# Optimization experiments

Measured on AMD Instinct MI355X. Metric: run time of the kernel, lower is better.

The kernel has to match this reference:

```python
import jax, jax.numpy as jnp
import numpy as np

N = 100000
IN_F, C1, C2, C3, OUT_F = 64, 64, 64, 64, 8


def setup_inputs() -> dict:
    key = jax.random.key(0)
    ks = jax.random.split(key, 12)
    x = jax.random.normal(ks[0], (N, IN_F), dtype=jnp.float32)
    edge_index = jax.random.randint(ks[1], (2, 1600000), 0, N, dtype=jnp.int64)

    def lin(kw, kb, fi, fo):
        s = 1.0 / np.sqrt(fi)
        W = jax.random.uniform(kw, (fi, fo), jnp.float32, -s, s)
        b = jax.random.uniform(kb, (fo,), jnp.float32, -s, s)
        return W, b

    W1, b1 = lin(ks[2], ks[3], IN_F, C1)
    W2, b2 = lin(ks[4], ks[5], C1, C2)
    W3, b3 = lin(ks[6], ks[7], C2, C3)
    Wl, bl = lin(ks[8], ks[9], C3, OUT_F)
    return {"x": x, "edge_index": edge_index, "W1": W1, "b1": b1,
            "W2": W2, "b2": b2, "W3": W3, "b3": b3, "Wl": Wl, "bl": bl}


def _gcn_norm(edge_index, n):
    # add self loops, compute symmetric normalization D^-1/2 A D^-1/2
    loops = jnp.arange(n, dtype=edge_index.dtype)
    src = jnp.concatenate([edge_index[0], loops])
    dst = jnp.concatenate([edge_index[1], loops])
    deg = jax.ops.segment_sum(jnp.ones_like(dst, dtype=jnp.float32), dst, num_segments=n)
    dis = jnp.where(deg > 0, jax.lax.rsqrt(deg), 0.0)
    norm = dis[src] * dis[dst]  # [E+N]
    return src, dst, norm


def _gcn_layer(h, W, b, src, dst, norm, n):
    h = h @ W                                   # [N, Fout] small GEMM
    msg = h[src] * norm[:, None]                # gather + scale, [E+N, Fout]
    agg = jax.ops.segment_sum(msg, dst, num_segments=n)  # scatter-add
    return agg + b


def reference(x, edge_index, W1, b1, W2, b2, W3, b3, Wl, bl):
    n = x.shape[0]
    src, dst, norm = _gcn_norm(edge_index, n)
    h = jax.nn.relu(_gcn_layer(x, W1, b1, src, dst, norm, n))
    h = jax.nn.relu(_gcn_layer(h, W2, b2, src, dst, norm, n))
    h = jax.nn.relu(_gcn_layer(h, W3, b3, src, dst, norm, n))
    return h @ Wl + bl
```

## Files before the change

kernel.cpp:

```cpp
#include <hip/hip_runtime.h>
#include <hip/hip_fp16.h>

#define F 64
#define CHUNK 2048
#define BN 512
#define BSHIFT 9
#define CAP 20480

typedef int v4i __attribute__((ext_vector_type(4)));
typedef float fx4 __attribute__((ext_vector_type(4)));
typedef float v2f __attribute__((ext_vector_type(2)));
typedef _Float16 h8f __attribute__((ext_vector_type(8)));

union FB8 { uint4 u; h8f h; };
union FX4P { fx4 v; v2f p[2]; };

__global__ __launch_bounds__(256) void k_blkcnt(const int* __restrict__ dst,
                                                int* __restrict__ blkcnt,
                                                int E, int NB, int NBKT) {
    __shared__ int lcnt[256];
    int b = blockIdx.x, t = threadIdx.x;
    lcnt[t] = 0;
    __syncthreads();
    const v4i* d4 = (const v4i*)dst;
    int g0 = (b * CHUNK) >> 2;
    int E4 = E >> 2;
#pragma unroll
    for (int k = 0; k < 2; ++k) {
        int gi = g0 + k * 256 + t;
        if (gi < E4) {
            v4i q = __builtin_nontemporal_load(d4 + gi);
            atomicAdd(&lcnt[q.x >> BSHIFT], 1);
            atomicAdd(&lcnt[q.y >> BSHIFT], 1);
            atomicAdd(&lcnt[q.z >> BSHIFT], 1);
            atomicAdd(&lcnt[q.w >> BSHIFT], 1);
        }
    }
    __syncthreads();
    if (t < NBKT) blkcnt[t * NB + b] = lcnt[t];
}

__global__ __launch_bounds__(256) void k_bktscan(const int* __restrict__ blkcnt,
                                                 int* __restrict__ blkoff,
                                                 int* __restrict__ bkttot, int NB) {
    __shared__ int s[256];
    __shared__ int running;
    int seg = blockIdx.x;
    int t = threadIdx.x;
    if (t == 0) running = 0;
    __syncthreads();
    for (int base = 0; base < NB; base += 256) {
        int i = base + t;
        int v = (i < NB) ? blkcnt[seg * NB + i] : 0;
        s[t] = v;
        __syncthreads();
        for (int off = 1; off < 256; off <<= 1) {
            int x = (t >= off) ? s[t - off] : 0;
            __syncthreads();
            s[t] += x;
            __syncthreads();
        }
        int rbase = running;
        if (i < NB) blkoff[seg * NB + i] = rbase + s[t] - v;
        int ctot = s[255];
        __syncthreads();
        if (t == 0) running = rbase + ctot;
        __syncthreads();
    }
    if (t == 0) bkttot[seg] = running;
}

__global__ void k_sb(const int* __restrict__ bkttot, int* __restrict__ sb, int NBKT) {
    __shared__ int s[256];
    int t = threadIdx.x;
    int v = (t < NBKT) ? bkttot[t] : 0;
    s[t] = v;
    __syncthreads();
    for (int off = 1; off < 256; off <<= 1) {
        int x = (t >= off) ? s[t - off] : 0;
        __syncthreads();
        s[t] += x;
        __syncthreads();
    }
    if (t < NBKT) sb[t] = s[t] - v;
    if (t == NBKT - 1) sb[NBKT] = s[t];
}

__global__ __launch_bounds__(256) void k_stage2(const int* __restrict__ src,
                                                const int* __restrict__ dst,
                                                const int* __restrict__ blkoff,
                                                const int* __restrict__ sb,
                                                unsigned* __restrict__ stage,
                                                int E, int NB, int NBKT) {
    __shared__ int lcnt[256];
    __shared__ int lbase[257];
    __shared__ int obase[256];
    __shared__ int s[256];
    __shared__ unsigned rec[CHUNK];
    __shared__ unsigned char binof[CHUNK];
    int b = blockIdx.x, t = threadIdx.x;
    lcnt[t] = 0;
    __syncthreads();
    const v4i* d4 = (const v4i*)dst;
    const v4i* s4 = (const v4i*)src;
    int g0 = (b * CHUNK) >> 2;
    int E4 = E >> 2;
    int myseg[8], myrank[8];
    unsigned myrec[8];
#pragma unroll
    for (int k = 0; k < 2; ++k) {
        int gi = g0 + k * 256 + t;
        bool ok = gi < E4;
        v4i qd = {0, 0, 0, 0}, qs = {0, 0, 0, 0};
        if (ok) {
            qd = __builtin_nontemporal_load(d4 + gi);
            qs = __builtin_nontemporal_load(s4 + gi);
        }
        int dd[4] = {qd.x, qd.y, qd.z, qd.w};
        int ss[4] = {qs.x, qs.y, qs.z, qs.w};
#pragma unroll
        for (int j = 0; j < 4; ++j) {
            int idx = k * 4 + j;
            myseg[idx] = -1;
            if (ok) {
                int sg = dd[j] >> BSHIFT;
                myseg[idx] = sg;
                myrank[idx] = atomicAdd(&lcnt[sg], 1);
                myrec[idx] = ((unsigned)(dd[j] & (BN - 1)) << 17) | (unsigned)ss[j];
            }
        }
    }
    __syncthreads();
    int v = lcnt[t];
    s[t] = v;
    __syncthreads();
    for (int off = 1; off < 256; off <<= 1) {
        int x = (t >= off) ? s[t - off] : 0;
        __syncthreads();
        s[t] += x;
        __syncthreads();
    }
    lbase[t] = s[t] - v;
    if (t == 255) lbase[256] = s[255];
    obase[t] = (t < NBKT) ? sb[t] + blkoff[t * NB + b] : 0;
    __syncthreads();
#pragma unroll
    for (int k = 0; k < 8; ++k) {
        if (myseg[k] >= 0) {
            int p = lbase[myseg[k]] + myrank[k];
            rec[p] = myrec[k];
            binof[p] = (unsigned char)myseg[k];
        }
    }
    __syncthreads();
    int tot = lbase[256];
    for (int j = t; j < tot; j += 256) {
        int sg = binof[j];
        stage[obase[sg] + (j - lbase[sg])] = rec[j];
    }
}

__global__ __launch_bounds__(1024) void k_bincount(const unsigned* __restrict__ stage,
                                                   const int* __restrict__ sb,
                                                   int* __restrict__ count,
                                                   float* __restrict__ dis,
                                                   int* __restrict__ padtot, int n) {
    __shared__ int lc[BN];
    int bkt = blockIdx.x, t = threadIdx.x;
    int nb0 = bkt << BSHIFT;
    if (t < BN) lc[t] = 0;
    __syncthreads();
    int r0 = sb[bkt], r1 = sb[bkt + 1];
    for (int j = r0 + t; j < r1; j += 1024) {
        unsigned r = stage[j];
        atomicAdd(&lc[r >> 17], 1);
    }
    __syncthreads();
    int pv = 0;
    if (t < BN) {
        int node = nb0 + t;
        int cv = lc[t];
        if (node < n) {
            count[node] = cv;
            dis[node] = rsqrtf((float)(cv + 1));
            pv = (cv + 3) & ~3;
        }
    }
    __syncthreads();
    if (t < BN) lc[t] = pv;
    __syncthreads();
    for (int off = 256; off > 0; off >>= 1) {
        if (t < off) lc[t] += lc[t + off];
        __syncthreads();
    }
    if (t == 0) padtot[bkt] = lc[0];
}

__global__ void k_sb2(const int* __restrict__ padtot, int* __restrict__ rbase,
                      int* __restrict__ row_start, int NBKT, int n) {
    __shared__ int s[256];
    int t = threadIdx.x;
    int v = (t < NBKT) ? padtot[t] : 0;
    s[t] = v;
    __syncthreads();
    for (int off = 1; off < 256; off <<= 1) {
        int x = (t >= off) ? s[t - off] : 0;
        __syncthreads();
        s[t] += x;
        __syncthreads();
    }
    if (t < NBKT) rbase[t] = s[t] - v;
    if (t == NBKT - 1) { rbase[NBKT] = s[t]; row_start[n] = s[t]; }
}

__global__ __launch_bounds__(512) void k_binfill(const unsigned* __restrict__ stage,
                                                 const int* __restrict__ sb,
                                                 const int* __restrict__ count,
                                                 const int* __restrict__ rbase,
                                                 int* __restrict__ row_start,
                                                 int* __restrict__ csr, int n) {
    __shared__ int lcur[BN];
    __shared__ int sc[BN];
    __shared__ int buf[CAP];
    int bkt = blockIdx.x, t = threadIdx.x;
    int nb0 = bkt << BSHIFT;
    int node = nb0 + t;
    int pv = (node < n) ? ((count[node] + 3) & ~3) : 0;
    sc[t] = pv;
    __syncthreads();
    for (int off = 1; off < BN; off <<= 1) {
        int x = (t >= off) ? sc[t - off] : 0;
        __syncthreads();
        sc[t] += x;
        __syncthreads();
    }
    int excl = sc[t] - pv;
    int w0 = rbase[bkt];
    int wlen = sc[BN - 1];
    lcur[t] = excl;
    if (node < n) row_start[node] = w0 + excl;
    for (int j = t; j < wlen && j < CAP; j += 512) buf[j] = n;
    __syncthreads();
    int r0 = sb[bkt], r1 = sb[bkt + 1];
    for (int j = r0 + t; j < r1; j += 512) {
        unsigned r = stage[j];
        int p = atomicAdd(&lcur[r >> 17], 1);
        if (p < CAP) buf[p] = (int)(r & 0x1FFFFu);
    }
    __syncthreads();
    for (int j = t; j < wlen && j < CAP; j += 512) csr[w0 + j] = buf[j];
}

__global__ void k_prep(const float4* __restrict__ x4, const float* __restrict__ dis,
                       uint2* __restrict__ hs, uint2* __restrict__ hs2, int n) {
    int i = blockIdx.x * blockDim.x + threadIdx.x;
    int tot = (n + 1) * 16;
    if (i < tot) {
        int row = i >> 4;
        float dv = 0.0f;
        float4 v = make_float4(0.f, 0.f, 0.f, 0.f);
        if (row < n) { dv = dis[row]; v = x4[i]; }
        __half2 h01 = __floats2half2_rn(dv * v.x, dv * v.y);
        __half2 h23 = __floats2half2_rn(dv * v.z, dv * v.w);
        uint2 u;
        u.x = *(unsigned*)&h01;
        u.y = *(unsigned*)&h23;
        hs[i] = u;
    } else if (i < tot + 16) {
        hs2[(size_t)n * 16 + (i - tot)] = make_uint2(0u, 0u);
    }
}

__global__ __launch_bounds__(256) void k_layer(const __half* __restrict__ hin,
        const float* __restrict__ W, const float* __restrict__ b,
        const int* __restrict__ row_start, const int* __restrict__ csr,
        const float* __restrict__ dis, __half* __restrict__ hout,
        int n, int scale_out) {
    __shared__ char lds_all[16384];
    int tid = threadIdx.x;
    int lane = tid & 63;
    int wv = tid >> 6;
    int r0 = (blockIdx.x * 4 + wv) << 4;
    if (r0 >= n) return;
    char* myLds = lds_all + (wv << 12);
    unsigned short* X16 = (unsigned short*)myLds;
    const uint4* h4 = (const uint4*)hin;

    int r_  = lane & 15;
    int g4  = lane >> 4;
    int q32 = lane >> 1;
    int c2  = lane & 1;

    int lo = row_start[r0 + r_];
    int hi = row_start[r0 + r_ + 1];
    int s0 = __shfl(lo, 0);
    int s4 = __shfl(hi, 15);
    int NBb = (s4 - s0 + 31) >> 5;
    unsigned deg = (unsigned)(hi - lo);

    fx4 acc0 = {0.f, 0.f, 0.f, 0.f};
    fx4 acc1 = acc0, acc2 = acc0, acc3 = acc0;

    auto getnode = [&](int i) -> int {
        if (i < NBb) {
            int slot = s0 + (i << 5) + q32;
            int nd = csr[slot];
            return (slot < s4) ? nd : n;
        }
        return (q32 < 16) ? (r0 + q32) : n;
    };

    int nd0 = getnode(0);
    int ba = nd0 * 8 + c2 * 4;
    uint4 G0 = h4[ba], G1 = h4[ba + 1], G2 = h4[ba + 2], G3 = h4[ba + 3];
    int ndn = getnode(1);

    int q0 = q32;
    int q1 = q32 ^ 8;
    int q2 = q32 ^ 16;
    int q3 = q32 ^ 24;

    for (int t = 0; t <= NBb; ++t) {
        int fb = c2 << 5;
#define PUT(J, GG) { \
    unsigned short* p = X16 + ((fb + 8 * (J)) << 5); \
    p[q0]       = (unsigned short)(GG.x); \
    p[32 + q0]  = (unsigned short)(GG.x >> 16); \
    p[64 + q1]  = (unsigned short)(GG.y); \
    p[96 + q1]  = (unsigned short)(GG.y >> 16); \
    p[128 + q2] = (unsigned short)(GG.z); \
    p[160 + q2] = (unsigned short)(GG.z >> 16); \
    p[192 + q3] = (unsigned short)(GG.w); \
    p[224 + q3] = (unsigned short)(GG.w >> 16); \
}
        PUT(0, G0) PUT(1, G1) PUT(2, G2) PUT(3, G3)
#undef PUT
        if (t < NBb) {
            int bb = ndn * 8 + c2 * 4;
            G0 = h4[bb]; G1 = h4[bb + 1]; G2 = h4[bb + 2]; G3 = h4[bb + 3];
            ndn = getnode(t + 2);
        }
        unsigned w[4];
        if (t < NBb) {
            unsigned u0 = (unsigned)(s0 + (t << 5) + (g4 << 3)) - (unsigned)lo;
#pragma unroll
            for (int jj = 0; jj < 4; ++jj)
                w[jj] = ((u0 + 2 * jj) < deg ? 0x3C00u : 0u) |
                        ((u0 + 2 * jj + 1) < deg ? 0x3C000000u : 0u);
        } else {
            int k0 = g4 << 3;
#pragma unroll
            for (int jj = 0; jj < 4; ++jj)
                w[jj] = ((k0 + 2 * jj) == r_ ? 0x3C00u : 0u) |
                        ((k0 + 2 * jj + 1) == r_ ? 0x3C000000u : 0u);
        }
        FB8 af; af.u = make_uint4(w[0], w[1], w[2], w[3]);
        const char* rb = myLds + ((r_ << 6) + ((g4 ^ ((r_ >> 1) & 3)) << 4));
        FB8 b0, b1, b2, b3;
        b0.u = *(const uint4*)(rb);
        b1.u = *(const uint4*)(rb + 1024);
        b2.u = *(const uint4*)(rb + 2048);
        b3.u = *(const uint4*)(rb + 3072);
        acc0 = __builtin_amdgcn_mfma_f32_16x16x32_f16(af.h, b0.h, acc0, 0, 0, 0);
        acc1 = __builtin_amdgcn_mfma_f32_16x16x32_f16(af.h, b1.h, acc1, 0, 0, 0);
        acc2 = __builtin_amdgcn_mfma_f32_16x16x32_f16(af.h, b2.h, acc2, 0, 0, 0);
        acc3 = __builtin_amdgcn_mfma_f32_16x16x32_f16(af.h, b3.h, acc3, 0, 0, 0);
    }

    float* T = (float*)myLds;
#define TSTORE(S, A) { \
    int fb_ = ((16 * (S) + r_) << 4) + (g4 << 2); \
    *(fx4*)(T + fb_) = A; }
    TSTORE(0, acc0) TSTORE(1, acc1) TSTORE(2, acc2) TSTORE(3, acc3)
#undef TSTORE

    float bb_ = b[lane];
    v2f yv2[8];
#pragma unroll
    for (int k = 0; k < 8; ++k) { yv2[k].x = 0.f; yv2[k].y = 0.f; }
    const float* Wp = W + lane;
#pragma unroll 4
    for (int f = 0; f < 64; ++f) {
        float w = Wp[f << 6];
        v2f wv; wv.x = w; wv.y = w;
        const float* Tf = T + (f << 4);
        FX4P d0, d1, d2, d3;
        d0.v = *(const fx4*)(Tf);
        d1.v = *(const fx4*)(Tf + 4);
        d2.v = *(const fx4*)(Tf + 8);
        d3.v = *(const fx4*)(Tf + 12);
        yv2[0] += d0.p[0] * wv;  yv2[1] += d0.p[1] * wv;
        yv2[2] += d1.p[0] * wv;  yv2[3] += d1.p[1] * wv;
        yv2[4] += d2.p[0] * wv;  yv2[5] += d2.p[1] * wv;
        yv2[6] += d3.p[0] * wv;  yv2[7] += d3.p[1] * wv;
    }

#pragma unroll
    for (int r = 0; r < 16; ++r) {
        float yvr = (r & 1) ? yv2[r >> 1].y : yv2[r >> 1].x;
        float dd = dis[r0 + r];
        float y = fmaxf(yvr * dd + bb_, 0.f);
        if (scale_out) y *= dd;
        hout[((size_t)(r0 + r) << 6) + lane] = __float2half(y);
    }
}

__global__ __launch_bounds__(256) void k_final(const __half* __restrict__ h,
                                               const float* __restrict__ Wl,
                                               const float* __restrict__ bl,
                                               float* __restrict__ out, int n) {
    __shared__ float Ws[F * 8];
    __shared__ float bs[8];
    int tid = threadIdx.x;
    Ws[tid] = Wl[tid];
    Ws[tid + 256] = Wl[tid + 256];
    if (tid < 8) bs[tid] = bl[tid];
    __syncthreads();
    int idx = blockIdx.x * 256 + tid;
    if (idx >= n * 8) return;
    int row = idx >> 3;
    int o = idx & 7;
    const __half* hr = h + (size_t)row * F;
    float acc = bs[o];
#pragma unroll
    for (int k = 0; k < F; ++k) acc = fmaf(__half2float(hr[k]), Ws[k * 8 + o], acc);
    out[idx] = acc;
}

extern "C" void kernel_launch(void* const* d_in, const int* in_sizes, int n_in,
                              void* d_out, int out_size, void* d_ws, size_t ws_size,
                              hipStream_t stream) {
    const float* x  = (const float*)d_in[0];
    const int*   ei = (const int*)d_in[1];
    const float* W1 = (const float*)d_in[2];
    const float* b1 = (const float*)d_in[3];
    const float* W2 = (const float*)d_in[4];
    const float* b2 = (const float*)d_in[5];
    const float* W3 = (const float*)d_in[6];
    const float* b3 = (const float*)d_in[7];
    const float* Wl = (const float*)d_in[8];
    const float* bl = (const float*)d_in[9];
    float* out = (float*)d_out;

    int n = in_sizes[0] / F;
    int E = in_sizes[1] / 2;
    const int* src = ei;
    const int* dst = ei + E;

    int np   = (n + 256) & ~255;
    int cap  = E + 3 * n + 64;
    int NB   = (E + CHUNK - 1) / CHUNK;
    int NBKT = (n + BN - 1) >> BSHIFT;

    int*      count     = (int*)d_ws;
    int*      row_start = count + np;
    int*      blkcnt    = row_start + np;
    int*      blkoff    = blkcnt + 256 * NB;
    int*      bkttot    = blkoff + 256 * NB;
    int*      sb        = bkttot + 256;
    int*      padtot    = sb + 272;
    int*      rbase     = padtot + 256;
    float*    dis       = (float*)(rbase + 272);
    unsigned* stage     = (unsigned*)(dis + np);
    int*      csr       = (int*)(stage + ((E + 3) & ~3));
    __half*   buf1      = (__half*)(csr + ((cap + 3) & ~3));
    __half*   buf2      = buf1 + (size_t)(n + 1) * F;

    k_blkcnt<<<NB, 256, 0, stream>>>(dst, blkcnt, E, NB, NBKT);

    k_bktscan<<<NBKT, 256, 0, stream>>>(blkcnt, blkoff, bkttot, NB);
    k_sb<<<1, 256, 0, stream>>>(bkttot, sb, NBKT);
    k_stage2<<<NB, 256, 0, stream>>>(src, dst, blkoff, sb, stage, E, NB, NBKT);

    k_bincount<<<NBKT, 1024, 0, stream>>>(stage, sb, count, dis, padtot, n);
    k_sb2<<<1, 256, 0, stream>>>(padtot, rbase, row_start, NBKT, n);

    k_binfill<<<NBKT, 512, 0, stream>>>(stage, sb, count, rbase, row_start, csr, n);

    k_prep<<<((n + 1) * 16 + 16 + 255) / 256, 256, 0, stream>>>(
        (const float4*)x, dis, (uint2*)buf1, (uint2*)buf2, n);

    int nb_l = (n + 63) / 64;
    k_layer<<<nb_l, 256, 0, stream>>>(buf1, W1, b1, row_start, csr, dis, buf2, n, 1);
    k_layer<<<nb_l, 256, 0, stream>>>(buf2, W2, b2, row_start, csr, dis, buf1, n, 1);
    k_layer<<<nb_l, 256, 0, stream>>>(buf1, W3, b3, row_start, csr, dis, buf2, n, 0);

    k_final<<<(n * 8 + 255) / 256, 256, 0, stream>>>(buf2, Wl, bl, out, n);
}
```

Measured before the change: 269.6 us.

## Double-buffer neighbor gathers in GCN layer and use 8-wave blocks

The aggregation loop in k_layer now keeps two sets of gathered feature registers (G and H) and alternates between them, so each wave has two iterations of global loads in flight ahead of the LDS transpose and MFMA work. Separately, the block size goes from 4 to 8 waves (512 threads, 32 KB LDS), with the grid halved to match. The goal is to hide gather latency better. The cost is higher register pressure, which together with the larger blocks may reduce occupancy.

```diff
diff --git a/kernel.cpp b/kernel.cpp
--- a/kernel.cpp
+++ b/kernel.cpp
@@ -271,16 +271,16 @@
     }
 }
 
-__global__ __launch_bounds__(256) void k_layer(const __half* __restrict__ hin,
+__global__ __launch_bounds__(512) void k_layer(const __half* __restrict__ hin,
         const float* __restrict__ W, const float* __restrict__ b,
         const int* __restrict__ row_start, const int* __restrict__ csr,
         const float* __restrict__ dis, __half* __restrict__ hout,
         int n, int scale_out) {
-    __shared__ char lds_all[16384];
+    __shared__ char lds_all[32768];
     int tid = threadIdx.x;
     int lane = tid & 63;
     int wv = tid >> 6;
-    int r0 = (blockIdx.x * 4 + wv) << 4;
+    int r0 = (blockIdx.x * 8 + wv) << 4;
     if (r0 >= n) return;
     char* myLds = lds_all + (wv << 12);
     unsigned short* X16 = (unsigned short*)myLds;
@@ -310,19 +310,13 @@
         return (q32 < 16) ? (r0 + q32) : n;
     };
 
-    int nd0 = getnode(0);
-    int ba = nd0 * 8 + c2 * 4;
-    uint4 G0 = h4[ba], G1 = h4[ba + 1], G2 = h4[ba + 2], G3 = h4[ba + 3];
-    int ndn = getnode(1);
-
     int q0 = q32;
     int q1 = q32 ^ 8;
     int q2 = q32 ^ 16;
     int q3 = q32 ^ 24;
-
-    for (int t = 0; t <= NBb; ++t) {
-        int fb = c2 << 5;
-#define PUT(J, GG) { \
+    const char* rb = myLds + ((r_ << 6) + ((g4 ^ ((r_ >> 1) & 3)) << 4));
+
+#define PUT1(J, GG) { \
     unsigned short* p = X16 + ((fb + 8 * (J)) << 5); \
     p[q0]       = (unsigned short)(GG.x); \
     p[32 + q0]  = (unsigned short)(GG.x >> 16); \
@@ -333,39 +327,62 @@
     p[192 + q3] = (unsigned short)(GG.w); \
     p[224 + q3] = (unsigned short)(GG.w >> 16); \
 }
-        PUT(0, G0) PUT(1, G1) PUT(2, G2) PUT(3, G3)
-#undef PUT
-        if (t < NBb) {
-            int bb = ndn * 8 + c2 * 4;
-            G0 = h4[bb]; G1 = h4[bb + 1]; G2 = h4[bb + 2]; G3 = h4[bb + 3];
-            ndn = getnode(t + 2);
-        }
-        unsigned w[4];
-        if (t < NBb) {
-            unsigned u0 = (unsigned)(s0 + (t << 5) + (g4 << 3)) - (unsigned)lo;
-#pragma unroll
-            for (int jj = 0; jj < 4; ++jj)
-                w[jj] = ((u0 + 2 * jj) < deg ? 0x3C00u : 0u) |
-                        ((u0 + 2 * jj + 1) < deg ? 0x3C000000u : 0u);
-        } else {
-            int k0 = g4 << 3;
-#pragma unroll
-            for (int jj = 0; jj < 4; ++jj)
-                w[jj] = ((k0 + 2 * jj) == r_ ? 0x3C00u : 0u) |
-                        ((k0 + 2 * jj + 1) == r_ ? 0x3C000000u : 0u);
-        }
-        FB8 af; af.u = make_uint4(w[0], w[1], w[2], w[3]);
-        const char* rb = myLds + ((r_ << 6) + ((g4 ^ ((r_ >> 1) & 3)) << 4));
-        FB8 b0, b1, b2, b3;
-        b0.u = *(const uint4*)(rb);
-        b1.u = *(const uint4*)(rb + 1024);
-        b2.u = *(const uint4*)(rb + 2048);
-        b3.u = *(const uint4*)(rb + 3072);
-        acc0 = __builtin_amdgcn_mfma_f32_16x16x32_f16(af.h, b0.h, acc0, 0, 0, 0);
-        acc1 = __builtin_amdgcn_mfma_f32_16x16x32_f16(af.h, b1.h, acc1, 0, 0, 0);
-        acc2 = __builtin_amdgcn_mfma_f32_16x16x32_f16(af.h, b2.h, acc2, 0, 0, 0);
-        acc3 = __builtin_amdgcn_mfma_f32_16x16x32_f16(af.h, b3.h, acc3, 0, 0, 0);
-    }
+
+#define SMFMA(TT) { \
+    unsigned w[4]; \
+    if ((TT) < NBb) { \
+        unsigned u0 = (unsigned)(s0 + ((TT) << 5) + (g4 << 3)) - (unsigned)lo; \
+        w[0] = ((u0     ) < deg ? 0x3C00u : 0u) | ((u0 + 1u) < deg ? 0x3C000000u : 0u); \
+        w[1] = ((u0 + 2u) < deg ? 0x3C00u : 0u) | ((u0 + 3u) < deg ? 0x3C000000u : 0u); \
+        w[2] = ((u0 + 4u) < deg ? 0x3C00u : 0u) | ((u0 + 5u) < deg ? 0x3C000000u : 0u); \
+        w[3] = ((u0 + 6u) < deg ? 0x3C00u : 0u) | ((u0 + 7u) < deg ? 0x3C000000u : 0u); \
+    } else { \
+        int k0 = g4 << 3; \
+        w[0] = ((k0    ) == r_ ? 0x3C00u : 0u) | ((k0 + 1) == r_ ? 0x3C000000u : 0u); \
+        w[1] = ((k0 + 2) == r_ ? 0x3C00u : 0u) | ((k0 + 3) == r_ ? 0x3C000000u : 0u); \
+        w[2] = ((k0 + 4) == r_ ? 0x3C00u : 0u) | ((k0 + 5) == r_ ? 0x3C000000u : 0u); \
+        w[3] = ((k0 + 6) == r_ ? 0x3C00u : 0u) | ((k0 + 7) == r_ ? 0x3C000000u : 0u); \
+    } \
+    FB8 af; af.u = make_uint4(w[0], w[1], w[2], w[3]); \
+    FB8 b0_, b1_, b2_, b3_; \
+    b0_.u = *(const uint4*)(rb); \
+    b1_.u = *(const uint4*)(rb + 1024); \
+    b2_.u = *(const uint4*)(rb + 2048); \
+    b3_.u = *(const uint4*)(rb + 3072); \
+    acc0 = __builtin_amdgcn_mfma_f32_16x16x32_f16(af.h, b0_.h, acc0, 0, 0, 0); \
+    acc1 = __builtin_amdgcn_mfma_f32_16x16x32_f16(af.h, b1_.h, acc1, 0, 0, 0); \
+    acc2 = __builtin_amdgcn_mfma_f32_16x16x32_f16(af.h, b2_.h, acc2, 0, 0, 0); \
+    acc3 = __builtin_amdgcn_mfma_f32_16x16x32_f16(af.h, b3_.h, acc3, 0, 0, 0); \
+}
+
+    uint4 G0, G1, G2, G3, H0, H1, H2, H3;
+    int nx;
+    {
+        int a0 = getnode(0);
+        int ba = a0 * 8 + c2 * 4;
+        G0 = h4[ba]; G1 = h4[ba + 1]; G2 = h4[ba + 2]; G3 = h4[ba + 3];
+        int a1 = getnode(1);
+        int bb = a1 * 8 + c2 * 4;
+        H0 = h4[bb]; H1 = h4[bb + 1]; H2 = h4[bb + 2]; H3 = h4[bb + 3];
+        nx = getnode(2);
+    }
+
+    for (int t = 0; ; t += 2) {
+        { int fb = c2 << 5; PUT1(0, G0) PUT1(1, G1) PUT1(2, G2) PUT1(3, G3) }
+        { int bb = nx * 8 + c2 * 4;
+          G0 = h4[bb]; G1 = h4[bb + 1]; G2 = h4[bb + 2]; G3 = h4[bb + 3];
+          nx = getnode(t + 3); }
+        SMFMA(t)
+        if (t + 1 > NBb) break;
+        { int fb = c2 << 5; PUT1(0, H0) PUT1(1, H1) PUT1(2, H2) PUT1(3, H3) }
+        { int bb = nx * 8 + c2 * 4;
+          H0 = h4[bb]; H1 = h4[bb + 1]; H2 = h4[bb + 2]; H3 = h4[bb + 3];
+          nx = getnode(t + 4); }
+        SMFMA(t + 1)
+        if (t + 2 > NBb) break;
+    }
+#undef PUT1
+#undef SMFMA
 
     float* T = (float*)myLds;
 #define TSTORE(S, A) { \
@@ -480,10 +497,10 @@
     k_prep<<<((n + 1) * 16 + 16 + 255) / 256, 256, 0, stream>>>(
         (const float4*)x, dis, (uint2*)buf1, (uint2*)buf2, n);
 
-    int nb_l = (n + 63) / 64;
-    k_layer<<<nb_l, 256, 0, stream>>>(buf1, W1, b1, row_start, csr, dis, buf2, n, 1);
-    k_layer<<<nb_l, 256, 0, stream>>>(buf2, W2, b2, row_start, csr, dis, buf1, n, 1);
-    k_layer<<<nb_l, 256, 0, stream>>>(buf1, W3, b3, row_start, csr, dis, buf2, n, 0);
+    int nb_l = (n + 127) / 128;
+    k_layer<<<nb_l, 512, 0, stream>>>(buf1, W1, b1, row_start, csr, dis, buf2, n, 1);
+    k_layer<<<nb_l, 512, 0, stream>>>(buf2, W2, b2, row_start, csr, dis, buf1, n, 1);
+    k_layer<<<nb_l, 512, 0, stream>>>(buf1, W3, b3, row_start, csr, dis, buf2, n, 0);
 
     k_final<<<(n * 8 + 255) / 256, 256, 0, stream>>>(buf2, Wl, bl, out, n);
 }
```

New measurement: 283.4 us. 5.1% more time.
